# Performance work log

Hardware: AMD Instinct MI355X
Metric: run time of the kernel (lower is better)

## Reference

```python
import jax, jax.numpy as jnp
import numpy as np

N_HEAD = 12


def setup_inputs() -> dict:
    key = jax.random.key(0)
    kx, kq, kk, kv = jax.random.split(key, 4)
    b, n, d = 2, 2048, 768
    x = jax.random.normal(kx, (b, n, d), dtype=jnp.float32)
    # nn.Linear weights stored as [d_out, d_in]; y = x @ W.T (no bias, qkv_bias=False)
    scale = 1.0 / np.sqrt(d)
    Wq = jax.random.normal(kq, (d, d), dtype=jnp.float32) * scale
    Wk = jax.random.normal(kk, (d, d), dtype=jnp.float32) * scale
    Wv = jax.random.normal(kv, (d, d), dtype=jnp.float32) * scale
    return {"x": x, "Wq": Wq, "Wk": Wk, "Wv": Wv}


def reference(x, Wq, Wk, Wv):
    b, n, d = x.shape
    h = N_HEAD
    hd = d // h
    # linear projections (bias=False): x @ W.T, then split heads -> [b, h, n, hd]
    q = (x @ Wq.T).reshape(b, n, h, hd).transpose(0, 2, 1, 3)
    k = (x @ Wk.T).reshape(b, n, h, hd).transpose(0, 2, 1, 3)
    v = (x @ Wv.T).reshape(b, n, h, hd).transpose(0, 2, 1, 3)
    # raw (unscaled!) attention scores, matching the source (no / sqrt(head_dim))
    scores = jnp.einsum('bhqd,bhkd->bhqk', q, k)  # [b, h, n, n]
    causal = jnp.tril(jnp.ones((n, n), dtype=bool))
    scores = jnp.where(causal, scores, -jnp.inf)
    weights = jax.nn.softmax(scores, axis=-1)
    out = jnp.einsum('bhqk,bhkd->bhqd', weights, v)  # [b, h, n, hd]
    return out.transpose(0, 2, 1, 3).reshape(b, n, d)
```

## Files before the change

### kernel.cpp

```cpp
#include <hip/hip_runtime.h>
#include <hip/hip_bf16.h>
#include <stdint.h>

#define Bsz 2
#define NT  2048
#define DM  768
#define NH  12
#define HD  64
#define MT  (Bsz * NT)
#define NCAT (3 * DM)

typedef float    f32x4  __attribute__((ext_vector_type(4)));
typedef float    f32x16 __attribute__((ext_vector_type(16)));
typedef short    s16x8  __attribute__((ext_vector_type(8)));
typedef _Float16 f16x8  __attribute__((ext_vector_type(8)));
typedef int      v2i    __attribute__((ext_vector_type(2)));

#define GLOBAL_AS __attribute__((address_space(1)))
#define SHARED_AS __attribute__((address_space(3)))

__device__ inline unsigned short f2h(float f) {
    union { _Float16 h; unsigned short u; } c; c.h = (_Float16)f; return c.u;
}
__device__ inline float h2f(unsigned short u) {
    union { unsigned short u; _Float16 h; } c; c.u = u; return (float)c.h;
}
__device__ inline f16x8 ldh(const short* p) {
    return __builtin_bit_cast(f16x8, *(const s16x8*)p);
}
__device__ inline int cvtpkh(float lo, float hi_) {
    int r;
    asm("v_cvt_pkrtz_f16_f32 %0, %1, %2" : "=v"(r) : "v"(lo), "v"(hi_));
    return r;
}
__device__ inline void plswap(int& a, int& b) {
    v2i r = __builtin_amdgcn_permlane32_swap(a, b, false, false);
    a = r[0]; b = r[1];
}
__device__ inline f16x8 mk8(int a, int b, int c, int d) {
    union { int i[4]; f16x8 v; } u;
    u.i[0] = a; u.i[1] = b; u.i[2] = c; u.i[3] = d;
    return u.v;
}
#define mfma32 __builtin_amdgcn_mfma_f32_32x32x16_f16
#define mfma16 __builtin_amdgcn_mfma_f32_16x16x32_f16


__global__ __launch_bounds__(256) void cvt_x_kernel(const float* __restrict__ x,
                                                    short* __restrict__ xf, int n8) {
    int i = blockIdx.x * blockDim.x + threadIdx.x;
    if (i >= n8) return;
    const float4* p = (const float4*)x + (size_t)i * 2;
    float4 a = p[0], b = p[1];
    float v[8] = {a.x, a.y, a.z, a.w, b.x, b.y, b.z, b.w};
    union { unsigned short s[8]; uint4 q; } H;
#pragma unroll
    for (int j = 0; j < 8; ++j) H.s[j] = f2h(v[j]);
    ((uint4*)xf)[i] = H.q;
}

__global__ __launch_bounds__(256) void cvt_w_kernel(const float* __restrict__ Wq,
                                                    const float* __restrict__ Wk,
                                                    const float* __restrict__ Wv,
                                                    short* __restrict__ Wf, int per8) {
    int i = blockIdx.x * blockDim.x + threadIdx.x;
    if (i >= 3 * per8) return;
    const float* src; int j;
    if (i < per8)          { src = Wq; j = i; }
    else if (i < 2 * per8) { src = Wk; j = i - per8; }
    else                   { src = Wv; j = i - 2 * per8; }
    const float4* p = (const float4*)src + (size_t)j * 2;
    float4 a = p[0], b = p[1];
    float v[8] = {a.x, a.y, a.z, a.w, b.x, b.y, b.z, b.w};
    union { unsigned short s[8]; uint4 q; } H;
#pragma unroll
    for (int t = 0; t < 8; ++t) H.s[t] = f2h(v[t]);
    ((uint4*)Wf)[i] = H.q;
}


#define BM 128
#define BK 32
#define KSTEPS (DM / BK)

__global__ __launch_bounds__(256, 2) void qkv_proj_kernel(
        const short* __restrict__ xf, const short* __restrict__ Wf,
        short* __restrict__ Qf, short* __restrict__ Kf, short* __restrict__ Vf) {
    __shared__ short lds[2][2][BM * BK];

    const int tid = threadIdx.x;
    const int w = tid >> 6, lane = tid & 63;
    const int l15 = lane & 15, lg = lane >> 4;
    const int wr = w >> 1, wc = w & 1;

    const int tile_m = blockIdx.x * BM;
    const int tile_n = blockIdx.y * BM;

    const int arr = w >> 1, hlf = w & 1;
    const int srow = lane >> 2;
    const int scol = (lane & 3) * 8;
    const short* gsrc = (arr == 0) ? xf + (size_t)tile_m * DM
                                   : Wf + (size_t)tile_n * DM;
    const short* gsrc_lane = gsrc + (size_t)(hlf * 64 + srow) * DM + scol;

    f32x4 zero4 = {0.f, 0.f, 0.f, 0.f};
    f32x4 acc[4][4];
#pragma unroll
    for (int i = 0; i < 4; ++i)
#pragma unroll
        for (int j = 0; j < 4; ++j) acc[i][j] = zero4;

    auto stage = [&](int buf, int kt) {
        const short* g = gsrc_lane + kt * BK;
#pragma unroll
        for (int j = 0; j < 4; ++j) {
            __builtin_amdgcn_global_load_lds(
                (const GLOBAL_AS void*)(g + (size_t)j * 16 * DM),
                (SHARED_AS void*)(&lds[buf][arr][(hlf * 64 + j * 16) * BK]),
                16, 0, 0);
        }
    };

    stage(0, 0);
    int cur = 0;
    for (int kt = 0; kt < KSTEPS; ++kt) {
        __syncthreads();
        if (kt + 1 < KSTEPS) stage(cur ^ 1, kt + 1);

        f16x8 a[4], b[4];
#pragma unroll
        for (int f = 0; f < 4; ++f) {
            a[f] = ldh(&lds[cur][0][(wr * 64 + f * 16 + l15) * BK + lg * 8]);
            b[f] = ldh(&lds[cur][1][(wc * 64 + f * 16 + l15) * BK + lg * 8]);
        }
#pragma unroll
        for (int mf = 0; mf < 4; ++mf)
#pragma unroll
            for (int nf = 0; nf < 4; ++nf)
                acc[mf][nf] = mfma16(a[mf], b[nf], acc[mf][nf], 0, 0, 0);
        cur ^= 1;
    }

    const int zq = tile_n / DM;
    const int ncol0 = tile_n % DM;
#pragma unroll
    for (int mf = 0; mf < 4; ++mf) {
#pragma unroll
        for (int nf = 0; nf < 4; ++nf) {
            int col = ncol0 + wc * 64 + nf * 16 + l15;
            int h = col >> 6, dh = col & 63;
            int m0 = tile_m + wr * 64 + mf * 16 + lg * 4;
            int b2 = m0 >> 11, nt0 = m0 & (NT - 1);
            int bh_ = b2 * NH + h;
            if (zq == 2) {
                union { short s[4]; short4 v; } pk;
#pragma unroll
                for (int r = 0; r < 4; ++r) pk.s[r] = (short)f2h(acc[mf][nf][r]);
                *(short4*)&Vf[((size_t)bh_ * HD + dh) * NT + nt0] = pk.v;
            } else {
                short* Hp = (zq == 0) ? Qf : Kf;
#pragma unroll
                for (int r = 0; r < 4; ++r) {
                    size_t oidx = ((size_t)bh_ * NT + nt0 + r) * HD + dh;
                    Hp[oidx] = (short)f2h(acc[mf][nf][r]);
                }
            }
        }
    }
}


#define QB  128
#define KVB 64
#define NQB (NT / QB)
#define SEGT 8
#define SLOTS 40

__global__ __launch_bounds__(256) void attn_part_kernel(const short* __restrict__ Qf,
                                                        const short* __restrict__ Kf,
                                                        const short* __restrict__ Vf,
                                                        short* __restrict__ Op,
                                                        float2* __restrict__ ml) {
    const int s = blockIdx.x;
    int qb, seg;
    if (s < 4)       { qb = s;                 seg = 0; }
    else if (s < 12) { qb = 4 + ((s - 4) >> 1);  seg = (s - 4) & 1; }
    else if (s < 24) { qb = 8 + (s - 12) / 3;    seg = (s - 12) % 3; }
    else             { qb = 12 + ((s - 24) >> 2); seg = (s - 24) & 3; }
    const int bh = blockIdx.y;
    const int slot = bh * SLOTS + s;
    const int tid = threadIdx.x;
    const int w = tid >> 6, lane = tid & 63;
    const int l31 = lane & 31, hi = lane >> 5;

    __shared__ __align__(16) short lds[2][2 * 4096];

    const size_t kvoff = (size_t)bh * NT * HD;
    const short* Kfb = Kf + kvoff;
    const short* Vb  = Vf + (size_t)bh * HD * NT;

    const short* sbase[4]; int sstr[4]; int sdof[4];
#pragma unroll
    for (int k = 0; k < 4; ++k) {
        int c = tid + 256 * k;
        int arr = c >> 9, idx = c & 511;
        int row = idx >> 3, ch = idx & 7;
        if (arr == 0) { sbase[k] = Kfb + (size_t)row * HD + ch * 8; sstr[k] = KVB * HD; }
        else          { sbase[k] = Vb + (size_t)row * NT + ch * 8;  sstr[k] = KVB; }
        sdof[k] = arr * 4096 + row * 64 + ((ch ^ (row & 7)) << 3);
    }

    const int q0w   = qb * QB + w * 32;
    const int qg    = q0w + l31;
    const int qmaxw = q0w + 31;

    f16x8 qf[4];
    const size_t qrow = kvoff + (size_t)qg * HD;
#pragma unroll
    for (int c = 0; c < 4; ++c) qf[c] = ldh(Qf + qrow + c * 16 + hi * 8);

    f32x16 o0{}, o1{};
    float m_run = -1e30f, l_run = 0.f;

    const int t0   = seg * SEGT;
    const int tend = min(t0 + SEGT, 2 * qb + 2);

    {
        uint4 ld0[4];
#pragma unroll
        for (int k = 0; k < 4; ++k) ld0[k] = *(const uint4*)(sbase[k] + (size_t)t0 * sstr[k]);
#pragma unroll
        for (int k = 0; k < 4; ++k) *(uint4*)(&lds[0][sdof[k]]) = ld0[k];
    }

    for (int t = t0; t < tend; ++t) {
        __syncthreads();
        const int cur = (t - t0) & 1;
        const int kv0 = t * KVB;
        const bool haveNext = (t + 1 < tend);
        uint4 ldn[4];
        if (haveNext) {
#pragma unroll
            for (int k = 0; k < 4; ++k)
                ldn[k] = *(const uint4*)(sbase[k] + (size_t)(t + 1) * sstr[k]);
        }

        if (kv0 <= qmaxw) {
            const short* Ks = &lds[cur][0];
            const short* Vs = &lds[cur][4096];
#pragma unroll
            for (int c2 = 0; c2 < 2; ++c2) {
                f32x16 S{};
                const int kvr = c2 * 32 + l31;
                const int swb = kvr * 64, sw7 = kvr & 7;
#pragma unroll
                for (int c = 0; c < 4; ++c) {
                    int off = swb + ((((c << 1) + hi) ^ sw7) << 3);
                    S = mfma32(ldh(&Ks[off]), qf[c], S, 0, 0, 0);
                }
                float p[16]; float pmax = -3e38f;
#pragma unroll
                for (int r = 0; r < 16; ++r) {
                    int kvg = kv0 + c2 * 32 + (r & 3) + 8 * (r >> 2) + 4 * hi;
                    float sv = (kvg > qg) ? -3e38f : S[r];
                    p[r] = sv;
                    pmax = fmaxf(pmax, sv);
                }
                pmax = fmaxf(pmax, __shfl_xor(pmax, 32));
                if (!__all(pmax - m_run <= 8.0f)) {
                    float mn = fmaxf(m_run, pmax);
                    float al = __expf(m_run - mn);
                    m_run = mn; l_run *= al;
                    int ai = __builtin_bit_cast(int, al);
#pragma unroll
                    for (int r = 0; r < 16; ++r) {
                        int kr = (r & 3) + 8 * (r >> 2) + 4 * hi;
                        float a = __builtin_bit_cast(float,
                                      __builtin_amdgcn_ds_bpermute(kr << 2, ai));
                        o0[r] *= a; o1[r] *= a;
                    }
                }
                float rs = 0.f;
#pragma unroll
                for (int r = 0; r < 16; ++r) { p[r] = __expf(p[r] - m_run); rs += p[r]; }
                rs += __shfl_xor(rs, 32);
                l_run += rs;
                int cpk[8];
#pragma unroll
                for (int i = 0; i < 8; ++i) cpk[i] = cvtpkh(p[2 * i], p[2 * i + 1]);
                int a0 = cpk[0], b0 = cpk[2]; plswap(a0, b0);
                int a1 = cpk[1], b1 = cpk[3]; plswap(a1, b1);
                int a2 = cpk[4], b2 = cpk[6]; plswap(a2, b2);
                int a3 = cpk[5], b3 = cpk[7]; plswap(a3, b3);
                f16x8 pf[2] = { mk8(a0, a1, b0, b1), mk8(a2, a3, b2, b3) };
#pragma unroll
                for (int kc = 0; kc < 2; ++kc) {
                    int chunk = c2 * 4 + kc * 2 + hi;
                    int off0 = l31 * 64 + ((chunk ^ (l31 & 7)) << 3);
                    int off1 = (32 + l31) * 64 + ((chunk ^ (l31 & 7)) << 3);
                    o0 = mfma32(pf[kc], ldh(&Vs[off0]), o0, 0, 0, 0);
                    o1 = mfma32(pf[kc], ldh(&Vs[off1]), o1, 0, 0, 0);
                }
            }
        }

        if (haveNext) {
#pragma unroll
            for (int k = 0; k < 4; ++k) *(uint4*)(&lds[cur ^ 1][sdof[k]]) = ldn[k];
        }
    }

    float inv = 1.0f / l_run;
    int ii = __builtin_bit_cast(int, inv);
    short* op = Op + (size_t)slot * (QB * HD);
#pragma unroll
    for (int r = 0; r < 16; ++r) {
        int kr = (r & 3) + 8 * (r >> 2) + 4 * hi;
        float iv = __builtin_bit_cast(float, __builtin_amdgcn_ds_bpermute(kr << 2, ii));
        short* orow = op + (w * 32 + kr) * HD;
        orow[l31]      = (short)f2h(o0[r] * iv);
        orow[32 + l31] = (short)f2h(o1[r] * iv);
    }
    if (hi == 0) {
        float2 v; v.x = m_run; v.y = l_run;
        ml[(size_t)slot * QB + w * 32 + l31] = v;
    }
}


__global__ __launch_bounds__(256) void combine_kernel(const short* __restrict__ Op,
                                                      const float2* __restrict__ ml,
                                                      float* __restrict__ out) {
    const int qb = blockIdx.x, bh = blockIdx.y;
    const int b = bh / NH, h = bh % NH;
    const int nseg = (qb >> 2) + 1;
    const int baseg[4] = {0, 4, 12, 24};
    const int sbase = baseg[qb >> 2] + (qb & 3) * nseg;
    const int row = threadIdx.x >> 1;
    const int c0 = (threadIdx.x & 1) * 32;

    float m[4], l[4];
    float M = -3e38f;
    for (int s2 = 0; s2 < nseg; ++s2) {
        float2 t = ml[((size_t)(bh * SLOTS + sbase + s2)) * QB + row];
        m[s2] = t.x; l[s2] = t.y;
        M = fmaxf(M, t.x);
    }
    float wgt[4], L = 0.f;
    for (int s2 = 0; s2 < nseg; ++s2) { wgt[s2] = l[s2] * __expf(m[s2] - M); L += wgt[s2]; }
    float invL = 1.0f / L;

    float acc[32];
#pragma unroll
    for (int j = 0; j < 32; ++j) acc[j] = 0.f;
    for (int s2 = 0; s2 < nseg; ++s2) {
        const short* oprow = Op + ((size_t)(bh * SLOTS + sbase + s2) * QB + row) * HD + c0;
        float wg = wgt[s2] * invL;
#pragma unroll
        for (int v = 0; v < 4; ++v) {
            f16x8 d = ldh(oprow + v * 8);
#pragma unroll
            for (int j = 0; j < 8; ++j)
                acc[v * 8 + j] += wg * (float)d[j];
        }
    }
    float* orow = out + ((size_t)(b * NT + qb * QB + row)) * DM + h * HD + c0;
#pragma unroll
    for (int j = 0; j < 32; ++j) orow[j] = acc[j];
}


extern "C" void kernel_launch(void* const* d_in, const int* in_sizes, int n_in,
                              void* d_out, int out_size, void* d_ws, size_t ws_size,
                              hipStream_t stream) {
    const float* x  = (const float*)d_in[0];
    const float* Wq = (const float*)d_in[1];
    const float* Wk = (const float*)d_in[2];
    const float* Wv = (const float*)d_in[3];
    float* outp = (float*)d_out;

    const size_t MD = (size_t)MT * DM;
    const size_t DD = (size_t)DM * DM;

    short* wsp = (short*)d_ws;
    short* xf = wsp;
    short* Wf = xf + MD;
    short* Qf = Wf + 3 * DD;
    short* Kf = Qf + MD;
    short* Vf = Kf + MD;
    short* Op = Vf + MD;
    float2* mlp = (float2*)(Op + (size_t)Bsz * NH * SLOTS * QB * HD);

    int n8x = (int)(MD / 8);
    cvt_x_kernel<<<dim3((n8x + 255) / 256), 256, 0, stream>>>(x, xf, n8x);
    int per8 = (int)(DD / 8);
    cvt_w_kernel<<<dim3((3 * per8 + 255) / 256), 256, 0, stream>>>(Wq, Wk, Wv, Wf, per8);
    qkv_proj_kernel<<<dim3(MT / BM, NCAT / BM), 256, 0, stream>>>(xf, Wf, Qf, Kf, Vf);
    attn_part_kernel<<<dim3(SLOTS, Bsz * NH), 256, 0, stream>>>(Qf, Kf, Vf, Op, mlp);
    combine_kernel<<<dim3(NQB, Bsz * NH), 256, 0, stream>>>(Op, mlp, outp);
}
```

Before: 164.8 us.

## Split attention into finer KV segments, use exp2 with prescaled Q, skip masked subtiles

Halves the KV segment length so the split-KV attention launches 72 work slots per head instead of 40, to spread the causal work more evenly across CUs. The partial-output buffer is split across two workspace regions, one of them reusing the now-dead x/W conversion area. Q is prescaled by log2(e) in the projection epilogue so softmax can use the native v_exp_f32 instruction, with the rescale threshold adjusted to match. Fully masked 32-wide subtiles are skipped, and the per-element mask is applied only on diagonal subtiles. The cost is more partial outputs for the combine kernel to read and merge, and slightly more complex indexing.

```diff
diff --git a/kernel.cpp b/kernel.cpp
--- a/kernel.cpp
+++ b/kernel.cpp
@@ -18,15 +18,18 @@
 
 #define GLOBAL_AS __attribute__((address_space(1)))
 #define SHARED_AS __attribute__((address_space(3)))
+#define LOG2E 1.44269504088896f
 
 __device__ inline unsigned short f2h(float f) {
     union { _Float16 h; unsigned short u; } c; c.h = (_Float16)f; return c.u;
 }
-__device__ inline float h2f(unsigned short u) {
-    union { unsigned short u; _Float16 h; } c; c.u = u; return (float)c.h;
-}
 __device__ inline f16x8 ldh(const short* p) {
     return __builtin_bit_cast(f16x8, *(const s16x8*)p);
+}
+__device__ inline float exp2i(float x) {
+    float r;
+    asm("v_exp_f32 %0, %1" : "=v"(r) : "v"(x));
+    return r;
 }
 __device__ inline int cvtpkh(float lo, float hi_) {
     int r;
@@ -159,10 +162,11 @@
                 *(short4*)&Vf[((size_t)bh_ * HD + dh) * NT + nt0] = pk.v;
             } else {
                 short* Hp = (zq == 0) ? Qf : Kf;
+                float scl = (zq == 0) ? LOG2E : 1.0f;
 #pragma unroll
                 for (int r = 0; r < 4; ++r) {
                     size_t oidx = ((size_t)bh_ * NT + nt0 + r) * HD + dh;
-                    Hp[oidx] = (short)f2h(acc[mf][nf][r]);
+                    Hp[oidx] = (short)f2h(acc[mf][nf][r] * scl);
                 }
             }
         }
@@ -173,22 +177,27 @@
 #define QB  128
 #define KVB 64
 #define NQB (NT / QB)
-#define SEGT 8
-#define SLOTS 40
+#define SEGT 4
+#define SLOTS 72
+#define OPA 600
+
+__device__ inline short* op_ptr(short* OpA_, short* OpB_, int g) {
+    return (g < OPA) ? OpA_ + (size_t)g * (QB * HD)
+                     : OpB_ + (size_t)(g - OPA) * (QB * HD);
+}
 
 __global__ __launch_bounds__(256) void attn_part_kernel(const short* __restrict__ Qf,
                                                         const short* __restrict__ Kf,
                                                         const short* __restrict__ Vf,
-                                                        short* __restrict__ Op,
+                                                        short* __restrict__ OpA_,
+                                                        short* __restrict__ OpB_,
                                                         float2* __restrict__ ml) {
-    const int s = blockIdx.x;
-    int qb, seg;
-    if (s < 4)       { qb = s;                 seg = 0; }
-    else if (s < 12) { qb = 4 + ((s - 4) >> 1);  seg = (s - 4) & 1; }
-    else if (s < 24) { qb = 8 + (s - 12) / 3;    seg = (s - 12) % 3; }
-    else             { qb = 12 + ((s - 24) >> 2); seg = (s - 24) & 3; }
+    int rem = blockIdx.x, a = 0;
+    while (rem >= 2 * (a + 1)) { rem -= 2 * (a + 1); ++a; }
+    const int qb  = 2 * a + (rem > a);
+    const int seg = (rem > a) ? rem - (a + 1) : rem;
     const int bh = blockIdx.y;
-    const int slot = bh * SLOTS + s;
+    const int g = bh * SLOTS + blockIdx.x;
     const int tid = threadIdx.x;
     const int w = tid >> 6, lane = tid & 63;
     const int l31 = lane & 31, hi = lane >> 5;
@@ -250,6 +259,8 @@
             const short* Vs = &lds[cur][4096];
 #pragma unroll
             for (int c2 = 0; c2 < 2; ++c2) {
+                const int kv0c = kv0 + c2 * 32;
+                if (kv0c > qmaxw) continue;
                 f32x16 S{};
                 const int kvr = c2 * 32 + l31;
                 const int swb = kvr * 64, sw7 = kvr & 7;
@@ -259,30 +270,35 @@
                     S = mfma32(ldh(&Ks[off]), qf[c], S, 0, 0, 0);
                 }
                 float p[16]; float pmax = -3e38f;
-#pragma unroll
-                for (int r = 0; r < 16; ++r) {
-                    int kvg = kv0 + c2 * 32 + (r & 3) + 8 * (r >> 2) + 4 * hi;
-                    float sv = (kvg > qg) ? -3e38f : S[r];
-                    p[r] = sv;
-                    pmax = fmaxf(pmax, sv);
+                if (kv0c + 31 > q0w) {
+#pragma unroll
+                    for (int r = 0; r < 16; ++r) {
+                        int kvg = kv0c + (r & 3) + 8 * (r >> 2) + 4 * hi;
+                        float sv = (kvg > qg) ? -3e38f : S[r];
+                        p[r] = sv;
+                        pmax = fmaxf(pmax, sv);
+                    }
+                } else {
+#pragma unroll
+                    for (int r = 0; r < 16; ++r) { p[r] = S[r]; pmax = fmaxf(pmax, S[r]); }
                 }
                 pmax = fmaxf(pmax, __shfl_xor(pmax, 32));
-                if (!__all(pmax - m_run <= 8.0f)) {
+                if (!__all(pmax - m_run <= 11.5416f)) {
                     float mn = fmaxf(m_run, pmax);
-                    float al = __expf(m_run - mn);
+                    float al = exp2i(m_run - mn);
                     m_run = mn; l_run *= al;
                     int ai = __builtin_bit_cast(int, al);
 #pragma unroll
                     for (int r = 0; r < 16; ++r) {
                         int kr = (r & 3) + 8 * (r >> 2) + 4 * hi;
-                        float a = __builtin_bit_cast(float,
+                        float av = __builtin_bit_cast(float,
                                       __builtin_amdgcn_ds_bpermute(kr << 2, ai));
-                        o0[r] *= a; o1[r] *= a;
+                        o0[r] *= av; o1[r] *= av;
                     }
                 }
                 float rs = 0.f;
 #pragma unroll
-                for (int r = 0; r < 16; ++r) { p[r] = __expf(p[r] - m_run); rs += p[r]; }
+                for (int r = 0; r < 16; ++r) { p[r] = exp2i(p[r] - m_run); rs += p[r]; }
                 rs += __shfl_xor(rs, 32);
                 l_run += rs;
                 int cpk[8];
@@ -312,7 +328,7 @@
 
     float inv = 1.0f / l_run;
     int ii = __builtin_bit_cast(int, inv);
-    short* op = Op + (size_t)slot * (QB * HD);
+    short* op = op_ptr(OpA_, OpB_, g);
 #pragma unroll
     for (int r = 0; r < 16; ++r) {
         int kr = (r & 3) + 8 * (r >> 2) + 4 * hi;
@@ -323,38 +339,46 @@
     }
     if (hi == 0) {
         float2 v; v.x = m_run; v.y = l_run;
-        ml[(size_t)slot * QB + w * 32 + l31] = v;
-    }
-}
-
-
-__global__ __launch_bounds__(256) void combine_kernel(const short* __restrict__ Op,
+        ml[(size_t)g * QB + w * 32 + l31] = v;
+    }
+}
+
+
+__global__ __launch_bounds__(256) void combine_kernel(const short* __restrict__ OpA_,
+                                                      const short* __restrict__ OpB_,
                                                       const float2* __restrict__ ml,
                                                       float* __restrict__ out) {
     const int qb = blockIdx.x, bh = blockIdx.y;
     const int b = bh / NH, h = bh % NH;
-    const int nseg = (qb >> 2) + 1;
-    const int baseg[4] = {0, 4, 12, 24};
-    const int sbase = baseg[qb >> 2] + (qb & 3) * nseg;
+    const int a = qb >> 1;
+    const int nseg = a + 1;
+    const int sbase = (a + 1) * (a + (qb & 1));
     const int row = threadIdx.x >> 1;
     const int c0 = (threadIdx.x & 1) * 32;
 
-    float m[4], l[4];
+    float m[8], l[8];
     float M = -3e38f;
     for (int s2 = 0; s2 < nseg; ++s2) {
         float2 t = ml[((size_t)(bh * SLOTS + sbase + s2)) * QB + row];
         m[s2] = t.x; l[s2] = t.y;
         M = fmaxf(M, t.x);
     }
-    float wgt[4], L = 0.f;
-    for (int s2 = 0; s2 < nseg; ++s2) { wgt[s2] = l[s2] * __expf(m[s2] - M); L += wgt[s2]; }
+    float wgt[8], L = 0.f;
+    for (int s2 = 0; s2 < nseg; ++s2) {
+        float e;
+        asm("v_exp_f32 %0, %1" : "=v"(e) : "v"(m[s2] - M));
+        wgt[s2] = l[s2] * e; L += wgt[s2];
+    }
     float invL = 1.0f / L;
 
     float acc[32];
 #pragma unroll
     for (int j = 0; j < 32; ++j) acc[j] = 0.f;
     for (int s2 = 0; s2 < nseg; ++s2) {
-        const short* oprow = Op + ((size_t)(bh * SLOTS + sbase + s2) * QB + row) * HD + c0;
+        int g = bh * SLOTS + sbase + s2;
+        const short* opg = (g < OPA) ? OpA_ + (size_t)g * (QB * HD)
+                                     : OpB_ + (size_t)(g - OPA) * (QB * HD);
+        const short* oprow = opg + (size_t)row * HD + c0;
         float wg = wgt[s2] * invL;
 #pragma unroll
         for (int v = 0; v < 4; ++v) {
@@ -388,14 +412,15 @@
     short* Qf = Wf + 3 * DD;
     short* Kf = Qf + MD;
     short* Vf = Kf + MD;
-    short* Op = Vf + MD;
-    float2* mlp = (float2*)(Op + (size_t)Bsz * NH * SLOTS * QB * HD);
+    short* OpA_ = wsp;
+    short* OpB_ = Vf + MD;
+    float2* mlp = (float2*)(OpB_ + (size_t)1128 * QB * HD);
 
     int n8x = (int)(MD / 8);
     cvt_x_kernel<<<dim3((n8x + 255) / 256), 256, 0, stream>>>(x, xf, n8x);
     int per8 = (int)(DD / 8);
     cvt_w_kernel<<<dim3((3 * per8 + 255) / 256), 256, 0, stream>>>(Wq, Wk, Wv, Wf, per8);
     qkv_proj_kernel<<<dim3(MT / BM, NCAT / BM), 256, 0, stream>>>(xf, Wf, Qf, Kf, Vf);
-    attn_part_kernel<<<dim3(SLOTS, Bsz * NH), 256, 0, stream>>>(Qf, Kf, Vf, Op, mlp);
-    combine_kernel<<<dim3(NQB, Bsz * NH), 256, 0, stream>>>(Op, mlp, outp);
-}
+    attn_part_kernel<<<dim3(SLOTS, Bsz * NH), 256, 0, stream>>>(Qf, Kf, Vf, OpA_, OpB_, mlp);
+    combine_kernel<<<dim3(NQB, Bsz * NH), 256, 0, stream>>>(OpA_, OpB_, mlp, outp);
+}
```

After: 165.5 us. About the same (+0.4%).
